# Optimization experiments

Measured on AMD Instinct MI355X. Metric: run time of the kernel, lower is better.

## Reference

```python
import jax, jax.numpy as jnp
import numpy as np

TOPK = 8
EPS = 1e-12  # matches torch F.normalize default eps


def setup_inputs() -> dict:
    key = jax.random.key(0)
    x = jax.random.normal(key, (8, 2048, 128), dtype=jnp.float32)
    return {"x": x}


def reference(x) -> jnp.ndarray:
    B, N, D = x.shape
    # --- pairwise dot scores on L2-normalized features (cosine similarity) ---
    norm = jnp.sqrt(jnp.sum(x * x, axis=-1, keepdims=True))
    normed = x / jnp.maximum(norm, EPS)
    scores = jnp.einsum('bnd,bmd->bnm', normed, normed)  # [B, N, N]

    # --- top-k per row -> binary adjacency via scatter ---
    _, idx = jax.lax.top_k(scores, TOPK)  # [B, N, k]
    bi = jnp.arange(B)[:, None, None]
    ni = jnp.arange(N)[None, :, None]
    adj = jnp.zeros((B, N, N), dtype=x.dtype).at[bi, ni, idx].set(1.0)

    # --- symmetrize and add self loops ---
    adj = jnp.maximum(adj, jnp.swapaxes(adj, 1, 2))
    eye = jnp.eye(N, dtype=x.dtype)
    adj = jnp.maximum(adj, eye[None, :, :])
    return adj
```

## Files before the change

### kernel.cpp

```cpp
#include <hip/hip_runtime.h>
#include <cstdint>

#define NN 2048
#define DD 128
#define BATCH 8
#define NROWS 16384
#define MARGIN 0.02f
#define CAP 64

typedef __attribute__((ext_vector_type(8))) short bf16x8;
typedef __attribute__((ext_vector_type(4))) float f32x4;
typedef unsigned long long u64;
typedef unsigned int u32;
typedef unsigned short u16;

__device__ __forceinline__ u32 bf16rne(float f) {
  u32 u = __float_as_uint(f);
  return (u + 0x7fffu + ((u >> 16) & 1u)) >> 16;
}

__global__ __launch_bounds__(256) void k_zero(float4* __restrict__ out, int n4) {
  int i = blockIdx.x * 256 + threadIdx.x;
  const int stride = gridDim.x * 256;
  const float4 z = {0.0f, 0.0f, 0.0f, 0.0f};
  for (; i < n4; i += stride) out[i] = z;
}

__global__ __launch_bounds__(256) void k_normalize(const float* __restrict__ x,
                                                   double* __restrict__ rinv,
                                                   u32* __restrict__ nb) {
  const int wave = threadIdx.x >> 6, lane = threadIdx.x & 63;
  const long long row = (long long)blockIdx.x * 4 + wave;
  float2 v = ((const float2*)(x + row * DD))[lane];
  const double d0 = v.x, d1 = v.y;
  double s = d0 * d0 + d1 * d1;
  #pragma unroll
  for (int m = 32; m >= 1; m >>= 1) s += __shfl_xor(s, m, 64);
  double den = sqrt(s); den = den > 1e-12 ? den : 1e-12;
  if (lane == 0) rinv[row] = 1.0 / den;
  double2 o; o.x = d0 / den; o.y = d1 / den;
  nb[row * (DD / 2) + lane] = bf16rne((float)o.x) | (bf16rne((float)o.y) << 16);
}

#define CXF(i, j) { const float a_ = L[i], b_ = L[j]; L[i] = fmaxf(a_, b_); L[j] = fminf(a_, b_); }
__device__ __forceinline__ void merge8f(float (&kv)[8], const float (&ov)[8]) {
  float L[8];
  #pragma unroll
  for (int i = 0; i < 8; ++i) L[i] = fmaxf(kv[i], ov[7 - i]);
  CXF(0, 4) CXF(1, 5) CXF(2, 6) CXF(3, 7)
  CXF(0, 2) CXF(1, 3) CXF(4, 6) CXF(5, 7)
  CXF(0, 1) CXF(2, 3) CXF(4, 5) CXF(6, 7)
  #pragma unroll
  for (int i = 0; i < 8; ++i) kv[i] = L[i];
}

__device__ __forceinline__ u64 make_key(double s, int col) {
  u64 u = (u64)__double_as_longlong(s);
  const u64 m = (u64)((long long)u >> 63);
  u ^= (m | 0x8000000000000000ull);
  return (u & ~2047ull) | (u64)(2047 - col);
}
__device__ __forceinline__ u64 umax64(u64 a, u64 b) { return a > b ? a : b; }
__device__ __forceinline__ u64 umin64(u64 a, u64 b) { return a > b ? b : a; }
__device__ __forceinline__ void merge8(u64 (&kv)[8], const u64 (&ov)[8]) {
  u64 L[8];
  #pragma unroll
  for (int i = 0; i < 8; ++i) L[i] = umax64(kv[i], ov[7 - i]);
#define CX(i, j) { const u64 a_ = L[i], b_ = L[j]; L[i] = umax64(a_, b_); L[j] = umin64(a_, b_); }
  CX(0, 4) CX(1, 5) CX(2, 6) CX(3, 7)
  CX(0, 2) CX(1, 3) CX(4, 6) CX(5, 7)
  CX(0, 1) CX(2, 3) CX(4, 5) CX(6, 7)
#undef CX
  #pragma unroll
  for (int i = 0; i < 8; ++i) kv[i] = L[i];
}
__device__ __forceinline__ void insert8u(u64 (&v)[8], u64 nk) {
  if (nk > v[7]) {
    v[7] = nk;
    #pragma unroll
    for (int q = 7; q >= 1; --q) {
      const u64 a = v[q - 1], b = v[q];
      const bool sw = b > a;
      v[q - 1] = sw ? b : a; v[q] = sw ? a : b;
    }
  }
}

__global__ __launch_bounds__(256) void k_gram(const u32* __restrict__ nb,
                                              u16* __restrict__ scores,
                                              u16* __restrict__ bmaxg) {
  __shared__ u16 bml[4][64][16];
  const int tid = threadIdx.x; const int w = tid >> 6; const int l = tid & 63;
  const int q = l >> 4; const int m = l & 15;
  bf16x8 pvals = {0,0,0,0,0,0,0,0}, pones = {0,0,0,0,0,0,0,0};
  if (q == 0) {
    pvals[0] = (short)(__float_as_uint((float)(m + 1)) >> 16);
    pones[0] = (short)(__float_as_uint(1.0f) >> 16);
  }
  const f32x4 z4 = {0.0f, 0.0f, 0.0f, 0.0f};
  const f32x4 pr  = __builtin_amdgcn_mfma_f32_16x16x32_bf16(pvals, pones, z4, 0, 0, 0);
  const f32x4 pr2 = __builtin_amdgcn_mfma_f32_16x16x32_bf16(pones, pvals, z4, 0, 0, 0);
  int cof[4];
  #pragma unroll
  for (int p = 0; p < 4; ++p) cof[p] = (int)pr[p] - 1;
  const int rof = (int)pr2[0] - 1;
  const bool contig = (cof[1] == cof[0] + 1) && (cof[2] == cof[0] + 2) &&
                      (cof[3] == cof[0] + 3) && ((cof[0] & 3) == 0);
  const int rowblk = blockIdx.x >> 2; const int split = blockIdx.x & 3;
  const int row0 = rowblk * 64;
  const int b = rowblk >> 5;
  const int c0w = split * 512 + w * 128;
  const u32* Bb = nb + ((long long)b * NN + c0w) * (DD / 2);

  bf16x8 ar4[4][4];
  #pragma unroll
  for (int rf = 0; rf < 4; ++rf) {
    const u32* Ap = nb + (long long)(row0 + 16 * rf + m) * (DD / 2) + 4 * q;
    #pragma unroll
    for (int cc = 0; cc < 4; ++cc) ar4[rf][cc] = *(const bf16x8*)(Ap + 16 * cc);
  }
  u16* rowb[4];
  #pragma unroll
  for (int rf = 0; rf < 4; ++rf)
    rowb[rf] = scores + (long long)(row0 + 16 * rf + rof) * NN + c0w;

  bf16x8 bcA[4], bcB[4];

#define LOADB(DST, T) { const u32* p_ = Bb + (long long)(16 * (T) + m) * (DD / 2) + 4 * q; \
  _Pragma("unroll") for (int cc = 0; cc < 4; ++cc) DST[cc] = *(const bf16x8*)(p_ + 16 * cc); }
#define STOREB(ACC, T, RF) { u16* sp = rowb[RF] + 16 * (T);                        \
    if (contig) {                                                                  \
      uint2 sv;                                                                    \
      sv.x = bf16rne(ACC[0]) | (bf16rne(ACC[1]) << 16);                            \
      sv.y = bf16rne(ACC[2]) | (bf16rne(ACC[3]) << 16);                            \
      *(uint2*)(sp + cof[0]) = sv;                                                 \
    } else {                                                                       \
      sp[cof[0]] = (u16)bf16rne(ACC[0]); sp[cof[1]] = (u16)bf16rne(ACC[1]);        \
      sp[cof[2]] = (u16)bf16rne(ACC[2]); sp[cof[3]] = (u16)bf16rne(ACC[3]);        \
    }                                                                              \
    float bm_ = fmaxf(fmaxf(ACC[0], ACC[1]), fmaxf(ACC[2], ACC[3]));               \
    bm_ = fmaxf(bm_, __shfl_xor(bm_, 16, 64));                                     \
    bm_ = fmaxf(bm_, __shfl_xor(bm_, 32, 64));                                     \
    if (q == 0) bml[w][16 * (RF) + m][T] = (u16)bf16rne(bm_); }
#define TILE(BC, T) {                                                              \
    _Pragma("unroll") for (int rf = 0; rf < 4; ++rf) {                             \
      f32x4 acc = z4;                                                              \
      _Pragma("unroll") for (int cc = 0; cc < 4; ++cc)                             \
        acc = __builtin_amdgcn_mfma_f32_16x16x32_bf16(BC[cc], ar4[rf][cc], acc, 0, 0, 0); \
      STOREB(acc, T, rf)                                                           \
    } }

  LOADB(bcA, 0)
  #pragma unroll
  for (int t = 0; t < 8; t += 2) {
    LOADB(bcB, t + 1)
    TILE(bcA, t)
    if (t + 2 < 8) LOADB(bcA, t + 2)
    TILE(bcB, t + 1)
  }
#undef LOADB
#undef STOREB
#undef TILE

  {
    const uint4 v = *(const uint4*)&bml[w][l][0];
    *(uint4*)(bmaxg + ((long long)split * 16384 + row0 + l) * 32 + w * 8) = v;
  }
}

__global__ __launch_bounds__(256) void k_topk_exact(const u16* __restrict__ scores,
                                                    const u16* __restrict__ bmaxg,
                                                    const float* __restrict__ x,
                                                    const double* __restrict__ rinv,
                                                    float* __restrict__ out) {
  __shared__ u32 scnt[4];
  __shared__ u32 sblkn[4];
  __shared__ u32 sblk[4][CAP];
  __shared__ u32 scand[4][CAP];

  const int w = threadIdx.x >> 6, l = threadIdx.x & 63;
  const int r = blockIdx.x * 4 + w;
  const int n = r & (NN - 1);
  const long long brow = r - n;

  if (l == 0) { scnt[w] = 0u; sblkn[w] = 0u; }

  const int s_ = l >> 4, idx_ = l & 15;
  const u32 bm2 = *(const u32*)(bmaxg + ((long long)s_ * 16384 + r) * 32 + 2 * idx_);
  const float b0 = __uint_as_float(bm2 << 16);
  const float b1 = __uint_as_float(bm2 & 0xFFFF0000u);
  const int blk0 = s_ * 32 + 2 * idx_;
  float mx = fmaxf(b0, b1);

  float kv8[8];
  {
    const float o  = __shfl_xor(mx, 1, 64);
    const float h2 = fmaxf(mx, o), l2 = fminf(mx, o);
    const float p0 = __shfl_xor(h2, 2, 64), p1 = __shfl_xor(l2, 2, 64);
    const float m0 = fmaxf(h2, p0);
    const float xx = fminf(h2, p0);
    const float yy = fmaxf(l2, p1);
    const float m3 = fminf(l2, p1);
    const float m1 = fmaxf(xx, yy);
    const float m2 = fminf(xx, yy);
    const float q0 = __shfl_xor(m0, 4, 64), q1 = __shfl_xor(m1, 4, 64);
    const float q2 = __shfl_xor(m2, 4, 64), q3 = __shfl_xor(m3, 4, 64);
    float L[8] = {m0, m1, m2, m3, q3, q2, q1, q0};
    CXF(0, 4) CXF(1, 5) CXF(2, 6) CXF(3, 7)
    CXF(0, 2) CXF(1, 3) CXF(4, 6) CXF(5, 7)
    CXF(0, 1) CXF(2, 3) CXF(4, 5) CXF(6, 7)
    #pragma unroll
    for (int s = 0; s < 8; ++s) kv8[s] = L[s];
    #pragma unroll
    for (int mk = 8; mk <= 32; mk <<= 1) {
      float ov[8];
      #pragma unroll
      for (int s = 0; s < 8; ++s) ov[s] = __shfl_xor(kv8[s], mk, 64);
      merge8f(kv8, ov);
    }
  }
  const float th = kv8[7] - MARGIN;

  if (b0 >= th) { const u32 id = atomicAdd(&sblkn[w], 1u); if (id < CAP) sblk[w][id] = (u32)blk0; }
  if (b1 >= th) { const u32 id = atomicAdd(&sblkn[w], 1u); if (id < CAP) sblk[w][id] = (u32)(blk0 + 1); }

  int c;
  const int nbq = (int)sblkn[w];
  const u16* rowp = scores + (long long)r * NN;
  if (nbq <= CAP) {
    for (int i = 0; i < nbq; i += 4) {
      const int bi = i + s_;
      const u32 blk = (bi < nbq) ? sblk[w][bi] : sblk[w][0];
      const int col = (int)blk * 16 + idx_;
      const float v = __uint_as_float((u32)rowp[col] << 16);
      if (bi < nbq && v >= th) {
        const u32 id = atomicAdd(&scnt[w], 1u);
        if (id < CAP) scand[w][id] = (u32)col;
      }
    }
    c = (int)scnt[w];
  } else {
    c = CAP + 1;
  }

  const float2 a2 = ((const float2*)(x + (long long)r * DD))[l];
  const double ri = rinv[r];
  u64 kv[8];
  #pragma unroll
  for (int s = 0; s < 8; ++s) kv[s] = 0ull;

  if (c <= CAP) {
    for (int i = 0; i < c; i += 4) {
      float2 vv[4]; int col[4];
      #pragma unroll
      for (int g = 0; g < 4; ++g) {
        const int idx = i + g;
        col[g] = (idx < c) ? ((int)scand[w][idx] & (NN - 1)) : 0;
        vv[g] = ((const float2*)(x + (brow + col[g]) * DD))[l];
      }
      #pragma unroll
      for (int g = 0; g < 4; ++g) {
        double d = fma((double)a2.x, (double)vv[g].x, (double)a2.y * (double)vv[g].y);
        #pragma unroll
        for (int mk = 1; mk <= 32; mk <<= 1) d += __shfl_xor(d, mk, 64);
        if (i + g < c) insert8u(kv, make_key(d * ri * rinv[brow + col[g]], col[g]));
      }
    }
  } else {
    for (int base = 0; base < NN; base += 64) {
      const int col = base + l;
      const float* ap = x + (long long)r * DD;
      const float* cp = x + (brow + col) * DD;
      double d = 0.0;
      for (int kk = 0; kk < 64; ++kk) {
        const float2 av = ((const float2*)ap)[kk];
        const float2 bv = ((const float2*)cp)[kk];
        d = fma((double)av.x, (double)bv.x, fma((double)av.y, (double)bv.y, d));
      }
      d = d * ri * rinv[brow + col];
      u64 one[8];
      one[0] = make_key(d, col);
      #pragma unroll
      for (int s = 1; s < 8; ++s) one[s] = 0ull;
      #pragma unroll
      for (int mk = 1; mk <= 32; mk <<= 1) {
        u64 ov[8];
        #pragma unroll
        for (int s = 0; s < 8; ++s) ov[s] = __shfl_xor(one[s], mk, 64);
        merge8(one, ov);
      }
      merge8(kv, one);
    }
  }

  const long long orow = (long long)r * NN;
  const long long obase = brow * NN;
  if (l == 8) out[orow + n] = 1.0f;
  #pragma unroll
  for (int s = 0; s < 8; ++s) {
    const int mcol = 2047 - (int)(kv[s] & 2047ull);
    if (l == s) {
      out[orow + mcol] = 1.0f;
      out[obase + (long long)mcol * NN + n] = 1.0f;
    }
  }
}

extern "C" void kernel_launch(void* const* d_in, const int* in_sizes, int n_in,
                              void* d_out, int out_size, void* d_ws, size_t ws_size,
                              hipStream_t stream) {
  const float* x = (const float*)d_in[0];
  float* out = (float*)d_out;
  char* ws = (char*)d_ws;
  u32* nb = (u32*)ws;
  double* rinv = (double*)(ws + 4194304);
  u16* scores = (u16*)(ws + 4325376);
  u16* bmaxg = (u16*)(ws + 71434240);

  hipLaunchKernelGGL(k_zero, dim3(4096), dim3(256), 0, stream,
                     (float4*)out, out_size / 4);
  hipLaunchKernelGGL(k_normalize, dim3(NROWS / 4), dim3(256), 0, stream, x, rinv, nb);
  hipLaunchKernelGGL(k_gram, dim3(1024), dim3(256), 0, stream, nb, scores, bmaxg);
  hipLaunchKernelGGL(k_topk_exact, dim3(NROWS / 4), dim3(256), 0, stream, scores, bmaxg, x, rinv, out);
}
```

Measured before the change: 254.3 us.

## Fuse output zeroing into gram kernel and split candidate dot products across quarter-waves

```diff
diff --git a/kernel.cpp b/kernel.cpp
--- a/kernel.cpp
+++ b/kernel.cpp
@@ -17,13 +17,6 @@
 __device__ __forceinline__ u32 bf16rne(float f) {
   u32 u = __float_as_uint(f);
   return (u + 0x7fffu + ((u >> 16) & 1u)) >> 16;
-}
-
-__global__ __launch_bounds__(256) void k_zero(float4* __restrict__ out, int n4) {
-  int i = blockIdx.x * 256 + threadIdx.x;
-  const int stride = gridDim.x * 256;
-  const float4 z = {0.0f, 0.0f, 0.0f, 0.0f};
-  for (; i < n4; i += stride) out[i] = z;
 }
 
 __global__ __launch_bounds__(256) void k_normalize(const float* __restrict__ x,
@@ -88,7 +81,8 @@
 
 __global__ __launch_bounds__(256) void k_gram(const u32* __restrict__ nb,
                                               u16* __restrict__ scores,
-                                              u16* __restrict__ bmaxg) {
+                                              u16* __restrict__ bmaxg,
+                                              float4* __restrict__ outz) {
   __shared__ u16 bml[4][64][16];
   const int tid = threadIdx.x; const int w = tid >> 6; const int l = tid & 63;
   const int q = l >> 4; const int m = l & 15;
@@ -166,6 +160,13 @@
     const uint4 v = *(const uint4*)&bml[w][l][0];
     *(uint4*)(bmaxg + ((long long)split * 16384 + row0 + l) * 32 + w * 8) = v;
   }
+
+  {
+    const int base = blockIdx.x * 256 + tid;
+    const float4 zf = {0.0f, 0.0f, 0.0f, 0.0f};
+    #pragma unroll 8
+    for (int k = 0; k < 32; ++k) outz[base + k * 262144] = zf;
+  }
 }
 
 __global__ __launch_bounds__(256) void k_topk_exact(const u16* __restrict__ scores,
@@ -243,28 +244,39 @@
     c = CAP + 1;
   }
 
-  const float2 a2 = ((const float2*)(x + (long long)r * DD))[l];
   const double ri = rinv[r];
   u64 kv[8];
   #pragma unroll
   for (int s = 0; s < 8; ++s) kv[s] = 0ull;
 
   if (c <= CAP) {
+    float2 a4[4];
+    #pragma unroll
+    for (int j = 0; j < 4; ++j)
+      a4[j] = ((const float2*)(x + (long long)r * DD))[idx_ + 16 * j];
+
     for (int i = 0; i < c; i += 4) {
-      float2 vv[4]; int col[4];
-      #pragma unroll
-      for (int g = 0; g < 4; ++g) {
-        const int idx = i + g;
-        col[g] = (idx < c) ? ((int)scand[w][idx] & (NN - 1)) : 0;
-        vv[g] = ((const float2*)(x + (brow + col[g]) * DD))[l];
+      const int gi = i + s_;
+      const bool valid = gi < c;
+      const int col = valid ? ((int)scand[w][gi] & (NN - 1)) : 0;
+      const float2* cp = (const float2*)(x + (brow + col) * DD);
+      double d = 0.0;
+      #pragma unroll
+      for (int j = 0; j < 4; ++j) {
+        const float2 bv = cp[idx_ + 16 * j];
+        d = fma((double)a4[j].x, (double)bv.x, d);
+        d = fma((double)a4[j].y, (double)bv.y, d);
       }
       #pragma unroll
-      for (int g = 0; g < 4; ++g) {
-        double d = fma((double)a2.x, (double)vv[g].x, (double)a2.y * (double)vv[g].y);
-        #pragma unroll
-        for (int mk = 1; mk <= 32; mk <<= 1) d += __shfl_xor(d, mk, 64);
-        if (i + g < c) insert8u(kv, make_key(d * ri * rinv[brow + col[g]], col[g]));
-      }
+      for (int mk = 1; mk <= 8; mk <<= 1) d += __shfl_xor(d, mk, 64);
+      if (valid) insert8u(kv, make_key(d * ri * rinv[brow + col], col));
+    }
+    #pragma unroll
+    for (int mk = 16; mk <= 32; mk <<= 1) {
+      u64 ov[8];
+      #pragma unroll
+      for (int s = 0; s < 8; ++s) ov[s] = __shfl_xor(kv[s], mk, 64);
+      merge8(kv, ov);
     }
   } else {
     for (int base = 0; base < NN; base += 64) {
@@ -317,9 +329,8 @@
   u16* scores = (u16*)(ws + 4325376);
   u16* bmaxg = (u16*)(ws + 71434240);
 
-  hipLaunchKernelGGL(k_zero, dim3(4096), dim3(256), 0, stream,
-                     (float4*)out, out_size / 4);
   hipLaunchKernelGGL(k_normalize, dim3(NROWS / 4), dim3(256), 0, stream, x, rinv, nb);
-  hipLaunchKernelGGL(k_gram, dim3(1024), dim3(256), 0, stream, nb, scores, bmaxg);
+  hipLaunchKernelGGL(k_gram, dim3(1024), dim3(256), 0, stream, nb, scores, bmaxg,
+                     (float4*)out);
   hipLaunchKernelGGL(k_topk_exact, dim3(NROWS / 4), dim3(256), 0, stream, scores, bmaxg, x, rinv, out);
 }
```

Result: faster. 248.1 us (-2.4%).
